# Performance work log

Hardware: AMD Instinct MI355X
Metric: run time of the kernel (lower is better)

Reference implementation:

```python
import jax, jax.numpy as jnp
import numpy as np

HIDDEN = 2048
N_HEADS = 32
N_KV_HEADS = 8
HEAD_DIM = HIDDEN // N_HEADS  # 64
KV_GROUPS = N_HEADS // N_KV_HEADS  # 4
ROPE_THETA = 10000.0
BSZ, SEQ = 2, 2048


def setup_inputs() -> dict:
    key = jax.random.key(0)
    ks = jax.random.split(key, 5)
    s = 0.02
    hidden_states = jax.random.normal(ks[0], (BSZ, SEQ, HIDDEN), jnp.float32)
    position_ids = jnp.broadcast_to(jnp.arange(SEQ, dtype=jnp.int32), (BSZ, SEQ))
    Wq = jax.random.normal(ks[1], (HIDDEN, HIDDEN), jnp.float32) * s
    Wk = jax.random.normal(ks[2], (N_KV_HEADS * HEAD_DIM, HIDDEN), jnp.float32) * s
    Wv = jax.random.normal(ks[3], (N_KV_HEADS * HEAD_DIM, HIDDEN), jnp.float32) * s
    Wo = jax.random.normal(ks[4], (HIDDEN, HIDDEN), jnp.float32) * s
    return {"hidden_states": hidden_states, "position_ids": position_ids,
            "Wq": Wq, "Wk": Wk, "Wv": Wv, "Wo": Wo}


def _rope_cos_sin(position_ids):
    # Llama rotary embedding: inv_freq over even dims, emb = [freqs, freqs]
    inv_freq = 1.0 / (ROPE_THETA ** (jnp.arange(0, HEAD_DIM, 2, dtype=jnp.float32) / HEAD_DIM))  # [Hd/2]
    freqs = position_ids.astype(jnp.float32)[..., None] * inv_freq  # [B, S, Hd/2]
    emb = jnp.concatenate([freqs, freqs], axis=-1)  # [B, S, Hd]
    return jnp.cos(emb), jnp.sin(emb)


def _rotate_half(x):
    x1, x2 = jnp.split(x, 2, axis=-1)
    return jnp.concatenate([-x2, x1], axis=-1)


def reference(hidden_states, position_ids, Wq, Wk, Wv, Wo):
    bsz, seq_len, _ = hidden_states.shape
    # projections (nn.Linear: y = x @ W.T)
    q = (hidden_states @ Wq.T).reshape(bsz, seq_len, N_HEADS, HEAD_DIM).transpose(0, 2, 1, 3)
    k = (hidden_states @ Wk.T).reshape(bsz, seq_len, N_KV_HEADS, HEAD_DIM).transpose(0, 2, 1, 3)
    v = (hidden_states @ Wv.T).reshape(bsz, seq_len, N_KV_HEADS, HEAD_DIM).transpose(0, 2, 1, 3)
    cos, sin = _rope_cos_sin(position_ids)  # [B, S, Hd]
    cos = cos[:, None, :, :]
    sin = sin[:, None, :, :]
    q = q * cos + _rotate_half(q) * sin
    k = k * cos + _rotate_half(k) * sin
    # GQA expand kv heads to full head count
    k = jnp.repeat(k, KV_GROUPS, axis=1)  # [B, H, S, Hd]
    v = jnp.repeat(v, KV_GROUPS, axis=1)
    # naive full-softmax attention (no causal mask, matching the source)
    scores = jnp.einsum('bhqd,bhkd->bhqk', q, k) / jnp.sqrt(jnp.float32(HEAD_DIM))
    attn_w = jax.nn.softmax(scores, axis=-1)
    attn_o = jnp.einsum('bhqk,bhkd->bhqd', attn_w, v)
    attn_o = attn_o.transpose(0, 2, 1, 3).reshape(bsz, seq_len, HIDDEN)
    return attn_o @ Wo.T
```

## Files before the change

### kernel.cpp

```cpp
#include <hip/hip_runtime.h>
#include <hip/hip_bf16.h>
#include <stdint.h>

#define HID 2048
#define NH 32
#define NKV 8
#define HD 64
#define BSZ 2
#define SEQ 2048
#define NROWS (BSZ*SEQ)
#define KVCOLS (NKV*HD)
#define QKVN 3072

typedef __attribute__((ext_vector_type(8))) short bf16x8;
typedef __attribute__((ext_vector_type(4))) float f32x4;
typedef __attribute__((ext_vector_type(16))) float f32x16;
typedef __attribute__((ext_vector_type(2))) unsigned int u32x2;

__device__ __forceinline__ unsigned short f2bf(float f) {
  union { float f; uint32_t u; } v; v.f = f;
  uint32_t r = v.u + 0x7FFFu + ((v.u >> 16) & 1u);
  return (unsigned short)(r >> 16);
}

__device__ __forceinline__ unsigned pack_bf16(float a, float b) {
  union { __hip_bfloat162 h; unsigned u; } cv;
  cv.h = __float22bfloat162_rn(make_float2(a, b));
  return cv.u;
}

__device__ __forceinline__ float sum16(const f32x16& s) {
  float a0 = s[0] + s[1], a1 = s[2] + s[3], a2 = s[4] + s[5], a3 = s[6] + s[7];
  float a4 = s[8] + s[9], a5 = s[10] + s[11], a6 = s[12] + s[13], a7 = s[14] + s[15];
  float b0 = a0 + a1, b1 = a2 + a3, b2 = a4 + a5, b3 = a6 + a7;
  return (b0 + b1) + (b2 + b3);
}

#define MKPB(S, B0) ({ \
  unsigned A_ = pack_bf16((S)[B0], (S)[(B0)+1]); \
  unsigned C_ = pack_bf16((S)[(B0)+2], (S)[(B0)+3]); \
  unsigned B_ = pack_bf16((S)[(B0)+4], (S)[(B0)+5]); \
  unsigned D_ = pack_bf16((S)[(B0)+6], (S)[(B0)+7]); \
  u32x2 r0_ = __builtin_amdgcn_permlane32_swap(A_, B_, false, false); \
  u32x2 r1_ = __builtin_amdgcn_permlane32_swap(C_, D_, false, false); \
  union { uint4 u; bf16x8 v; } cv_; \
  cv_.u.x = r0_.x; cv_.u.y = r1_.x; cv_.u.z = r0_.y; cv_.u.w = r1_.y; \
  cv_.v; })

#define ROPE_C (-0.41524101186092029f)
#define QSCL 0.18033688011112042f

#define C0 2097152
#define C1 3145728
#define C2 3407872
#define C3 3670016
#define CT 4718592
#define CT2 (CT + 32768)
__global__ __launch_bounds__(256) void cvt_all(
    const float* __restrict__ hs, const float* __restrict__ wq,
    const float* __restrict__ wk, const float* __restrict__ wv,
    const float* __restrict__ wo, const int* __restrict__ pos_ids,
    unsigned short* __restrict__ xb, unsigned short* __restrict__ wqkv,
    unsigned short* __restrict__ wob, float2* __restrict__ tab) {
  int i4 = blockIdx.x * 256 + threadIdx.x;
  const int stride = gridDim.x * 256;
  for (; i4 < CT2; i4 += stride) {
    if (i4 >= CT) {
      const int idx = i4 - CT;
      const int row = idx >> 3, jb = (idx & 7) * 4;
      const float pos = (float)pos_ids[row];
      float2 e[4];
      #pragma unroll
      for (int jj = 0; jj < 4; ++jj) {
        float sn, cs;
        __sincosf(pos * exp2f((float)(jb + jj) * ROPE_C), &sn, &cs);
        e[jj].x = cs; e[jj].y = sn;
      }
      *(float4*)(tab + (size_t)row * 32 + jb)     = *(const float4*)&e[0];
      *(float4*)(tab + (size_t)row * 32 + jb + 2) = *(const float4*)&e[2];
      continue;
    }
    const float* src; unsigned short* dst;
    if (i4 < C0)      { src = hs + (size_t)i4 * 4;            dst = xb   + (size_t)i4 * 4; }
    else if (i4 < C1) { src = wq + (size_t)(i4 - C0) * 4;     dst = wqkv + (size_t)(i4 - C0) * 4; }
    else if (i4 < C2) { src = wk + (size_t)(i4 - C1) * 4;     dst = wqkv + 4194304 + (size_t)(i4 - C1) * 4; }
    else if (i4 < C3) { src = wv + (size_t)(i4 - C2) * 4;     dst = wqkv + 5242880 + (size_t)(i4 - C2) * 4; }
    else              { src = wo + (size_t)(i4 - C3) * 4;     dst = wob  + (size_t)(i4 - C3) * 4; }
    float4 v = *(const float4*)src;
    ushort4 o;
    o.x = f2bf(v.x); o.y = f2bf(v.y); o.z = f2bf(v.z); o.w = f2bf(v.w);
    *(ushort4*)dst = o;
  }
}

#define BM 128
#define BN 128
#define BK 32

__global__ __launch_bounds__(256) void gemm_btn(
    const unsigned short* __restrict__ A,
    const unsigned short* __restrict__ B,
    float* __restrict__ C,
    int M, int N, int K)
{
  __shared__ unsigned short As[2][BM * BK];
  __shared__ unsigned short Bs[2][BN * BK];
  const int t = threadIdx.x;
  const int w = t >> 6, l = t & 63;
  const int wr = w >> 1, wc = w & 1;

  const int nwg = gridDim.x * gridDim.y;
  const int lin = blockIdx.y * gridDim.x + blockIdx.x;
  const int swz = (lin & 7) * (nwg >> 3) + (lin >> 3);
  const int bx = swz % gridDim.x, by = swz / gridDim.x;

  const int row0 = by * BM, col0 = bx * BN;
  const int lr = l & 15, lk = (l >> 4) * 8;

  f32x4 acc[4][4];
  for (int i = 0; i < 4; ++i)
    for (int j = 0; j < 4; ++j)
      acc[i][j] = (f32x4){0.f, 0.f, 0.f, 0.f};

  auto stage = [&](int bi, int k0) {
    #pragma unroll
    for (int i = 0; i < 2; ++i) {
      int ebase = i * 2048 + w * 512;
      int e = ebase + l * 8;
      const unsigned short* srcA = A + (size_t)(row0 + (e >> 5)) * K + k0 + (e & 31);
      const unsigned short* srcB = B + (size_t)(col0 + (e >> 5)) * K + k0 + (e & 31);
      __builtin_amdgcn_global_load_lds((const __attribute__((address_space(1))) void*)srcA,
          (__attribute__((address_space(3))) void*)&As[bi][ebase], 16, 0, 0);
      __builtin_amdgcn_global_load_lds((const __attribute__((address_space(1))) void*)srcB,
          (__attribute__((address_space(3))) void*)&Bs[bi][ebase], 16, 0, 0);
    }
  };

  stage(0, 0);
  __syncthreads();
  int bi = 0;
  for (int k0 = 0; k0 < K; k0 += BK) {
    if (k0 + BK < K) stage(bi ^ 1, k0 + BK);
    bf16x8 a[4], b[4];
    #pragma unroll
    for (int mi = 0; mi < 4; ++mi)
      a[mi] = *(const bf16x8*)&As[bi][(wr * 64 + mi * 16 + lr) * BK + lk];
    #pragma unroll
    for (int ni = 0; ni < 4; ++ni)
      b[ni] = *(const bf16x8*)&Bs[bi][(wc * 64 + ni * 16 + lr) * BK + lk];
    #pragma unroll
    for (int mi = 0; mi < 4; ++mi)
      #pragma unroll
      for (int ni = 0; ni < 4; ++ni)
        acc[mi][ni] = __builtin_amdgcn_mfma_f32_16x16x32_bf16(a[mi], b[ni], acc[mi][ni], 0, 0, 0);
    __syncthreads();
    bi ^= 1;
  }

  const int crow = (l >> 4) * 4, ccol = l & 15;
  #pragma unroll
  for (int mi = 0; mi < 4; ++mi)
    #pragma unroll
    for (int ni = 0; ni < 4; ++ni) {
      float* cp = C + (size_t)(row0 + wr * 64 + mi * 16 + crow) * N + col0 + wc * 64 + ni * 16 + ccol;
      #pragma unroll
      for (int r = 0; r < 4; ++r)
        cp[(size_t)r * N] = acc[mi][ni][r];
    }
}

__global__ __launch_bounds__(256) void gemm_qkv(
    const unsigned short* __restrict__ A,
    const unsigned short* __restrict__ B,
    const float2* __restrict__ tab,
    unsigned short* __restrict__ Qb,
    unsigned short* __restrict__ Kb,
    unsigned short* __restrict__ Vt)
{
  __shared__ unsigned short Sh[4 * BM * BK];
  unsigned short* As = Sh;
  unsigned short* Bs = Sh + 2 * BM * BK;
  const int t = threadIdx.x;
  const int w = t >> 6, l = t & 63;
  const int wr = w >> 1, wc = w & 1;

  const int nwg = gridDim.x * gridDim.y;
  const int lin = blockIdx.y * gridDim.x + blockIdx.x;
  const int swz = (lin & 7) * (nwg >> 3) + (lin >> 3);
  const int bx = swz % gridDim.x, by = swz / gridDim.x;

  const int row0 = by * BM, col0 = bx * BN;
  const int lr = l & 15, lk = (l >> 4) * 8;

  f32x4 acc[4][4];
  for (int i = 0; i < 4; ++i)
    for (int j = 0; j < 4; ++j)
      acc[i][j] = (f32x4){0.f, 0.f, 0.f, 0.f};

  auto stage = [&](int bi, int k0) {
    #pragma unroll
    for (int i = 0; i < 2; ++i) {
      int ebase = i * 2048 + w * 512;
      int e = ebase + l * 8;
      const unsigned short* srcA = A + (size_t)(row0 + (e >> 5)) * HID + k0 + (e & 31);
      const unsigned short* srcB = B + (size_t)(col0 + (e >> 5)) * HID + k0 + (e & 31);
      __builtin_amdgcn_global_load_lds((const __attribute__((address_space(1))) void*)srcA,
          (__attribute__((address_space(3))) void*)&As[bi * BM * BK + ebase], 16, 0, 0);
      __builtin_amdgcn_global_load_lds((const __attribute__((address_space(1))) void*)srcB,
          (__attribute__((address_space(3))) void*)&Bs[bi * BM * BK + ebase], 16, 0, 0);
    }
  };

  stage(0, 0);
  __syncthreads();
  int bi = 0;
  for (int k0 = 0; k0 < HID; k0 += BK) {
    if (k0 + BK < HID) stage(bi ^ 1, k0 + BK);
    bf16x8 a[4], b[4];
    #pragma unroll
    for (int mi = 0; mi < 4; ++mi)
      a[mi] = *(const bf16x8*)&As[bi * BM * BK + (wr * 64 + mi * 16 + lr) * BK + lk];
    #pragma unroll
    for (int ni = 0; ni < 4; ++ni)
      b[ni] = *(const bf16x8*)&Bs[bi * BM * BK + (wc * 64 + ni * 16 + lr) * BK + lk];
    #pragma unroll
    for (int mi = 0; mi < 4; ++mi)
      #pragma unroll
      for (int ni = 0; ni < 4; ++ni)
        acc[mi][ni] = __builtin_amdgcn_mfma_f32_16x16x32_bf16(a[mi], b[ni], acc[mi][ni], 0, 0, 0);
    __syncthreads();
    bi ^= 1;
  }

  const int crow = (l >> 4) * 4, ccol = l & 15;
  const int colbase = col0 + wc * 64;
  const int b = row0 >> 11;
  const int s0row = (row0 + wr * 64) & (SEQ - 1);
  char* Tw = (char*)Sh + w * 8192;
  const int dl = l >> 3, sg = l & 7;

  if (colbase < HID + KVCOLS) {
    const bool isQ = colbase < HID;
    const float scl = isQ ? QSCL : 1.0f;
    const int hh = (isQ ? colbase : colbase - HID) >> 6;
    unsigned short* base = (isQ ? Qb + ((size_t)(b * NH + hh) * SEQ) * HD
                                : Kb + ((size_t)(b * NKV + hh) * SEQ) * HD);
    #pragma unroll
    for (int mi = 0; mi < 4; ++mi) {
      const int rowb = row0 + wr * 64 + mi * 16 + crow;
      #pragma unroll
      for (int r = 0; r < 4; ++r) {
        const int row = rowb + r;
        const int sl = mi * 16 + crow + r;
        const int xsw = (sl & 7) << 4;
        const float2* tr = tab + (size_t)row * 32 + ccol;
        #pragma unroll
        for (int ni = 0; ni < 2; ++ni) {
          const float2 cssn = tr[ni * 16];
          const float x1 = acc[mi][ni][r], x2 = acc[mi][ni + 2][r];
          const int d1 = (ni * 16 + ccol) * 2;
          *(unsigned short*)(Tw + ((sl * 128 + d1) ^ xsw)) =
              f2bf((x1 * cssn.x - x2 * cssn.y) * scl);
          *(unsigned short*)(Tw + ((sl * 128 + d1 + 64) ^ xsw)) =
              f2bf((x2 * cssn.x + x1 * cssn.y) * scl);
        }
      }
    }
    asm volatile("s_waitcnt lgkmcnt(0)" ::: "memory");
    __builtin_amdgcn_sched_barrier(0);
    #pragma unroll
    for (int dg = 0; dg < 8; ++dg) {
      const int sl = dg * 8 + dl;
      uint4 v = *(const uint4*)(Tw + ((sl * 128 + sg * 16) ^ ((sl & 7) << 4)));
      *(uint4*)(base + (size_t)(s0row + sl) * HD + sg * 8) = v;
    }
  } else {
    const int cv = colbase - (HID + KVCOLS);
    const int kh = cv >> 6;
    unsigned short* vbase = Vt + ((size_t)(b * NKV + kh) * HD) * SEQ;
    #pragma unroll
    for (int ni = 0; ni < 4; ++ni) {
      const int d = ni * 16 + ccol;
      #pragma unroll
      for (int mi = 0; mi < 4; ++mi) {
        const int sl = mi * 16 + crow;
        ushort4 o;
        o.x = f2bf(acc[mi][ni][0]);
        o.y = f2bf(acc[mi][ni][1]);
        o.z = f2bf(acc[mi][ni][2]);
        o.w = f2bf(acc[mi][ni][3]);
        *(ushort4*)(Tw + ((d * 128 + sl * 2) ^ ((d & 7) << 4))) = o;
      }
    }
    asm volatile("s_waitcnt lgkmcnt(0)" ::: "memory");
    __builtin_amdgcn_sched_barrier(0);
    #pragma unroll
    for (int dg = 0; dg < 8; ++dg) {
      const int d = dg * 8 + dl;
      uint4 v = *(const uint4*)(Tw + ((d * 128 + sg * 16) ^ ((d & 7) << 4)));
      *(uint4*)(vbase + (size_t)d * SEQ + s0row + sg * 8) = v;
    }
  }
}

__global__ __launch_bounds__(512, 4) void attn_kernel(
    const unsigned short* __restrict__ Qb,
    const unsigned short* __restrict__ Kb,
    const unsigned short* __restrict__ Vt,
    unsigned short* __restrict__ AO)
{
  __shared__ unsigned short Ks[2][64 * 64];
  __shared__ unsigned short Vs[2][64 * 64];

  const int lin = blockIdx.x;
  const int bid = (lin & 7) * 64 + (lin >> 3);
  const int qtile = bid & 7;
  const int h = (bid >> 3) & 31;
  const int b = bid >> 8;
  const int kh = h >> 2;
  const int t = threadIdx.x, w = t >> 6, l = t & 63;
  const int lq = l & 31, hi = l >> 5;
  const int sw = (lq & 7) << 4;
  const int qrow = qtile * 256 + w * 32 + lq;

  bf16x8 qf[4];
  {
    const unsigned short* Qrow = Qb + ((size_t)(b * NH + h) * SEQ + qrow) * HD;
    #pragma unroll
    for (int dk = 0; dk < 4; ++dk)
      qf[dk] = *(const bf16x8*)(Qrow + dk * 16 + hi * 8);
  }

  const unsigned short* Kt  = Kb + (size_t)(b * NKV + kh) * SEQ * HD;
  const unsigned short* Vth = Vt + (size_t)(b * NKV + kh) * HD * SEQ;

  const int dest = t * 16;
  const int srow = dest >> 7;
  const int scol = dest & 127;
  const int wdest = dest ^ ((srow & 7) << 4);
  const char* KsrcBase = (const char*)Kt + dest;
  const char* VsrcBase = (const char*)(Vth + (size_t)srow * SEQ) + scol;

  uint4 kreg, vreg;
  auto issue = [&](int kv0) {
    kreg = *(const uint4*)(KsrcBase + (size_t)kv0 * 128);
    vreg = *(const uint4*)(VsrcBase + kv0 * 2);
  };
  auto lwrite = [&](int si) {
    *(uint4*)((char*)Ks[si] + wdest) = kreg;
    *(uint4*)((char*)Vs[si] + wdest) = vreg;
  };

  const f32x16 Z = {0,0,0,0,0,0,0,0,0,0,0,0,0,0,0,0};
  float lsum = 0.f;
  f32x16 o0 = Z, o1 = Z;

  issue(0);
  lwrite(0);
  __syncthreads();

  int bi = 0;
  for (int it = 0; it < SEQ / 64; ++it) {
    const bool more = (it + 1 < SEQ / 64);
    if (more) issue((it + 1) * 64);

    const char* Kp = (const char*)Ks[bi];
    const char* Vp = (const char*)Vs[bi];

    f32x16 s0, s1;
    __builtin_amdgcn_s_setprio(1);
    {
      bf16x8 kf0 = *(const bf16x8*)(Kp + lq * 128 + ((hi * 16) ^ sw));
      bf16x8 kf1 = *(const bf16x8*)(Kp + 4096 + lq * 128 + ((hi * 16) ^ sw));
      s0 = __builtin_amdgcn_mfma_f32_32x32x16_bf16(kf0, qf[0], Z, 0, 0, 0);
      s1 = __builtin_amdgcn_mfma_f32_32x32x16_bf16(kf1, qf[0], Z, 0, 0, 0);
    }
    #pragma unroll
    for (int dk = 1; dk < 4; ++dk) {
      const int cb = dk * 32 + hi * 16;
      bf16x8 kf0 = *(const bf16x8*)(Kp + lq * 128 + (cb ^ sw));
      bf16x8 kf1 = *(const bf16x8*)(Kp + 4096 + lq * 128 + (cb ^ sw));
      s0 = __builtin_amdgcn_mfma_f32_32x32x16_bf16(kf0, qf[dk], s0, 0, 0, 0);
      s1 = __builtin_amdgcn_mfma_f32_32x32x16_bf16(kf1, qf[dk], s1, 0, 0, 0);
    }
    __builtin_amdgcn_s_setprio(0);

    #pragma unroll
    for (int r = 0; r < 16; ++r) { s0[r] = exp2f(s0[r]); s1[r] = exp2f(s1[r]); }
    float rs = sum16(s0) + sum16(s1);
    rs += __shfl_xor(rs, 32);
    lsum += rs;

    bf16x8 pb0 = MKPB(s0, 0), pb1 = MKPB(s0, 8), pb2 = MKPB(s1, 0), pb3 = MKPB(s1, 8);

    __builtin_amdgcn_s_setprio(1);
    #pragma unroll
    for (int ks = 0; ks < 4; ++ks) {
      const int cb = ks * 32 + hi * 16;
      bf16x8 vf0 = *(const bf16x8*)(Vp + lq * 128 + (cb ^ sw));
      bf16x8 vf1 = *(const bf16x8*)(Vp + 4096 + lq * 128 + (cb ^ sw));
      bf16x8 pa = (ks == 0) ? pb0 : (ks == 1) ? pb1 : (ks == 2) ? pb2 : pb3;
      o0 = __builtin_amdgcn_mfma_f32_32x32x16_bf16(vf0, pa, o0, 0, 0, 0);
      o1 = __builtin_amdgcn_mfma_f32_32x32x16_bf16(vf1, pa, o1, 0, 0, 0);
    }
    __builtin_amdgcn_s_setprio(0);

    if (more) lwrite(bi ^ 1);
    __syncthreads();
    bi ^= 1;
  }

  const float inv = 1.0f / lsum;
  unsigned short* op = AO + ((size_t)(b * SEQ) + qrow) * HID + h * 64;
  #pragma unroll
  for (int r = 0; r < 16; r += 2) {
    const int d = (r & 3) + 8 * (r >> 2) + 4 * hi;
    *(unsigned*)(op + d)      = pack_bf16(o0[r] * inv, o0[r + 1] * inv);
    *(unsigned*)(op + 32 + d) = pack_bf16(o1[r] * inv, o1[r + 1] * inv);
  }
}

extern "C" void kernel_launch(void* const* d_in, const int* in_sizes, int n_in,
                              void* d_out, int out_size, void* d_ws, size_t ws_size,
                              hipStream_t stream) {
  const float* hs  = (const float*)d_in[0];
  const int*   pos = (const int*)d_in[1];
  const float* Wq  = (const float*)d_in[2];
  const float* Wk  = (const float*)d_in[3];
  const float* Wv  = (const float*)d_in[4];
  const float* Wo  = (const float*)d_in[5];
  float* out = (float*)d_out;

  char* ws = (char*)d_ws;
  size_t off = 0;
  auto carve = [&](size_t bytes) { void* p = ws + off; off += (bytes + 255) & ~(size_t)255; return p; };

  unsigned short* Xb    = (unsigned short*)carve((size_t)NROWS * HID * 2);
  unsigned short* Wqkvb = (unsigned short*)carve((size_t)QKVN * HID * 2);
  unsigned short* Wob   = (unsigned short*)carve((size_t)HID * HID * 2);
  unsigned short* Qbh   = (unsigned short*)carve((size_t)NROWS * HID * 2);
  unsigned short* Kbh   = (unsigned short*)carve((size_t)NROWS * KVCOLS * 2);
  unsigned short* Vtb   = (unsigned short*)carve((size_t)NROWS * KVCOLS * 2);
  unsigned short* AO    = (unsigned short*)carve((size_t)NROWS * HID * 2);
  float2*         Tab   = (float2*)carve((size_t)NROWS * 32 * sizeof(float2));

  cvt_all<<<2048, 256, 0, stream>>>(hs, Wq, Wk, Wv, Wo, pos, Xb, Wqkvb, Wob, Tab);

  gemm_qkv<<<dim3(QKVN / BN, NROWS / BM), 256, 0, stream>>>(Xb, Wqkvb, Tab, Qbh, Kbh, Vtb);

  attn_kernel<<<BSZ * NH * (SEQ / 256), 512, 0, stream>>>(Qbh, Kbh, Vtb, AO);

  gemm_btn<<<dim3(HID / BN, NROWS / BM), 256, 0, stream>>>(AO, Wob, out, NROWS, HID, HID);
}
```

Before: 260.0 us.

## Rewrite projection GEMMs with 256x256 tiles, BK=64, swizzled LDS and 8-wave blocks

```diff
diff --git a/kernel.cpp b/kernel.cpp
--- a/kernel.cpp
+++ b/kernel.cpp
@@ -49,6 +49,10 @@
 
 #define ROPE_C (-0.41524101186092029f)
 #define QSCL 0.18033688011112042f
+
+#define GLOAD(src, dst) __builtin_amdgcn_global_load_lds( \
+    (const __attribute__((address_space(1))) void*)(src), \
+    (__attribute__((address_space(3))) void*)(dst), 16, 0, 0)
 
 #define C0 2097152
 #define C1 3145728
@@ -93,83 +97,108 @@
   }
 }
 
-#define BM 128
-#define BN 128
-#define BK 32
-
-__global__ __launch_bounds__(256) void gemm_btn(
+#define G_STAGE8(bufB, ktn) \
+  { \
+    _Pragma("unroll") \
+    for (int j = 0; j < 4; ++j) { \
+      int d = wcn * 4096 + j * 1024 + l * 16; \
+      int colp = (d & 127) ^ (((d >> 7) & 7) << 4); \
+      GLOAD((const char*)A + (size_t)(row0 + wr * 128 + (d >> 7)) * 4096 + (ktn) * 128 + colp, \
+            SL + (bufB) + wr * 16384 + d); \
+    } \
+    _Pragma("unroll") \
+    for (int j = 0; j < 4; ++j) { \
+      int d = (wr * 2 + (wcn & 1)) * 4096 + j * 1024 + l * 16; \
+      int colp = (d & 127) ^ (((d >> 7) & 7) << 4); \
+      GLOAD((const char*)B + (size_t)(col0 + (wcn >> 1) * 128 + (d >> 7)) * 4096 + (ktn) * 128 + colp, \
+            SL + (bufB) + 32768 + (wcn >> 1) * 16384 + d); \
+    } \
+  }
+
+#define G_TILE(bufB) \
+  _Pragma("unroll") \
+  for (int ks = 0; ks < 2; ++ks) { \
+    bf16x8 af[8]; \
+    _Pragma("unroll") \
+    for (int mi = 0; mi < 8; ++mi) \
+      af[mi] = *(const bf16x8*)(SL + (bufB) + ABb + mi * 2048 + laneK[ks]); \
+    _Pragma("unroll") \
+    for (int nh = 0; nh < 2; ++nh) { \
+      bf16x8 b0 = *(const bf16x8*)(SL + (bufB) + BBb + (nh * 2) * 2048 + laneK[ks]); \
+      bf16x8 b1 = *(const bf16x8*)(SL + (bufB) + BBb + (nh * 2 + 1) * 2048 + laneK[ks]); \
+      __builtin_amdgcn_s_barrier(); \
+      __builtin_amdgcn_sched_barrier(0); \
+      __builtin_amdgcn_s_setprio(1); \
+      _Pragma("unroll") \
+      for (int mi = 0; mi < 8; ++mi) { \
+        acc[mi][nh * 2]     = __builtin_amdgcn_mfma_f32_16x16x32_bf16(af[mi], b0, acc[mi][nh * 2], 0, 0, 0); \
+        acc[mi][nh * 2 + 1] = __builtin_amdgcn_mfma_f32_16x16x32_bf16(af[mi], b1, acc[mi][nh * 2 + 1], 0, 0, 0); \
+      } \
+      __builtin_amdgcn_s_setprio(0); \
+      __builtin_amdgcn_s_barrier(); \
+      __builtin_amdgcn_sched_barrier(0); \
+    } \
+  }
+
+#define G_PREAMBLE \
+  __shared__ char SL[131072]; \
+  const int t = threadIdx.x; \
+  const int w = t >> 6, l = t & 63; \
+  const int wr = w >> 2, wcn = w & 3; \
+  const int lr = l & 15, lk2 = (l >> 4) * 16; \
+  const int sw7 = (lr & 7) << 4; \
+  const int nwg = gridDim.x * gridDim.y; \
+  const int lin = blockIdx.y * gridDim.x + blockIdx.x; \
+  const int swzb = (lin & 7) * (nwg >> 3) + (lin >> 3); \
+  const int bx = swzb % gridDim.x, by = swzb / gridDim.x; \
+  const int row0 = by * 256, col0 = bx * 256; \
+  int laneK[2]; \
+  laneK[0] = lr * 128 + (lk2 ^ sw7); \
+  laneK[1] = lr * 128 + ((64 + lk2) ^ sw7); \
+  const int ABb = wr * 16384; \
+  const int BBb = 32768 + (wcn >> 1) * 16384 + (wcn & 1) * 8192; \
+  f32x4 acc[8][4]; \
+  _Pragma("unroll") \
+  for (int i = 0; i < 8; ++i) \
+    _Pragma("unroll") \
+    for (int j = 0; j < 4; ++j) acc[i][j] = (f32x4){0.f, 0.f, 0.f, 0.f}; \
+  G_STAGE8(0, 0); \
+  asm volatile("s_waitcnt vmcnt(0)" ::: "memory"); \
+  __syncthreads(); \
+  _Pragma("unroll 1") \
+  for (int kt2 = 0; kt2 < 16; ++kt2) { \
+    const int kt = kt2 * 2; \
+    if (kt + 1 < 32) G_STAGE8(65536, kt + 1); \
+    G_TILE(0); \
+    asm volatile("s_waitcnt vmcnt(0)" ::: "memory"); \
+    __builtin_amdgcn_s_barrier(); \
+    __builtin_amdgcn_sched_barrier(0); \
+    if (kt + 2 < 32) G_STAGE8(0, kt + 2); \
+    G_TILE(65536); \
+    asm volatile("s_waitcnt vmcnt(0)" ::: "memory"); \
+    __builtin_amdgcn_s_barrier(); \
+    __builtin_amdgcn_sched_barrier(0); \
+  }
+
+__global__ __launch_bounds__(512, 2) void gemm_btn256(
     const unsigned short* __restrict__ A,
     const unsigned short* __restrict__ B,
-    float* __restrict__ C,
-    int M, int N, int K)
+    float* __restrict__ C)
 {
-  __shared__ unsigned short As[2][BM * BK];
-  __shared__ unsigned short Bs[2][BN * BK];
-  const int t = threadIdx.x;
-  const int w = t >> 6, l = t & 63;
-  const int wr = w >> 1, wc = w & 1;
-
-  const int nwg = gridDim.x * gridDim.y;
-  const int lin = blockIdx.y * gridDim.x + blockIdx.x;
-  const int swz = (lin & 7) * (nwg >> 3) + (lin >> 3);
-  const int bx = swz % gridDim.x, by = swz / gridDim.x;
-
-  const int row0 = by * BM, col0 = bx * BN;
-  const int lr = l & 15, lk = (l >> 4) * 8;
-
-  f32x4 acc[4][4];
-  for (int i = 0; i < 4; ++i)
-    for (int j = 0; j < 4; ++j)
-      acc[i][j] = (f32x4){0.f, 0.f, 0.f, 0.f};
-
-  auto stage = [&](int bi, int k0) {
-    #pragma unroll
-    for (int i = 0; i < 2; ++i) {
-      int ebase = i * 2048 + w * 512;
-      int e = ebase + l * 8;
-      const unsigned short* srcA = A + (size_t)(row0 + (e >> 5)) * K + k0 + (e & 31);
-      const unsigned short* srcB = B + (size_t)(col0 + (e >> 5)) * K + k0 + (e & 31);
-      __builtin_amdgcn_global_load_lds((const __attribute__((address_space(1))) void*)srcA,
-          (__attribute__((address_space(3))) void*)&As[bi][ebase], 16, 0, 0);
-      __builtin_amdgcn_global_load_lds((const __attribute__((address_space(1))) void*)srcB,
-          (__attribute__((address_space(3))) void*)&Bs[bi][ebase], 16, 0, 0);
-    }
-  };
-
-  stage(0, 0);
-  __syncthreads();
-  int bi = 0;
-  for (int k0 = 0; k0 < K; k0 += BK) {
-    if (k0 + BK < K) stage(bi ^ 1, k0 + BK);
-    bf16x8 a[4], b[4];
-    #pragma unroll
-    for (int mi = 0; mi < 4; ++mi)
-      a[mi] = *(const bf16x8*)&As[bi][(wr * 64 + mi * 16 + lr) * BK + lk];
-    #pragma unroll
-    for (int ni = 0; ni < 4; ++ni)
-      b[ni] = *(const bf16x8*)&Bs[bi][(wc * 64 + ni * 16 + lr) * BK + lk];
-    #pragma unroll
-    for (int mi = 0; mi < 4; ++mi)
-      #pragma unroll
-      for (int ni = 0; ni < 4; ++ni)
-        acc[mi][ni] = __builtin_amdgcn_mfma_f32_16x16x32_bf16(a[mi], b[ni], acc[mi][ni], 0, 0, 0);
-    __syncthreads();
-    bi ^= 1;
-  }
-
+  G_PREAMBLE
   const int crow = (l >> 4) * 4, ccol = l & 15;
   #pragma unroll
-  for (int mi = 0; mi < 4; ++mi)
+  for (int mi = 0; mi < 8; ++mi)
     #pragma unroll
     for (int ni = 0; ni < 4; ++ni) {
-      float* cp = C + (size_t)(row0 + wr * 64 + mi * 16 + crow) * N + col0 + wc * 64 + ni * 16 + ccol;
+      float* cp = C + (size_t)(row0 + wr * 128 + mi * 16 + crow) * HID + col0 + wcn * 64 + ni * 16 + ccol;
       #pragma unroll
       for (int r = 0; r < 4; ++r)
-        cp[(size_t)r * N] = acc[mi][ni][r];
-    }
-}
-
-__global__ __launch_bounds__(256) void gemm_qkv(
+        cp[(size_t)r * HID] = acc[mi][ni][r];
+    }
+}
+
+__global__ __launch_bounds__(512, 2) void gemm_qkv256(
     const unsigned short* __restrict__ A,
     const unsigned short* __restrict__ B,
     const float2* __restrict__ tab,
@@ -177,67 +206,12 @@
     unsigned short* __restrict__ Kb,
     unsigned short* __restrict__ Vt)
 {
-  __shared__ unsigned short Sh[4 * BM * BK];
-  unsigned short* As = Sh;
-  unsigned short* Bs = Sh + 2 * BM * BK;
-  const int t = threadIdx.x;
-  const int w = t >> 6, l = t & 63;
-  const int wr = w >> 1, wc = w & 1;
-
-  const int nwg = gridDim.x * gridDim.y;
-  const int lin = blockIdx.y * gridDim.x + blockIdx.x;
-  const int swz = (lin & 7) * (nwg >> 3) + (lin >> 3);
-  const int bx = swz % gridDim.x, by = swz / gridDim.x;
-
-  const int row0 = by * BM, col0 = bx * BN;
-  const int lr = l & 15, lk = (l >> 4) * 8;
-
-  f32x4 acc[4][4];
-  for (int i = 0; i < 4; ++i)
-    for (int j = 0; j < 4; ++j)
-      acc[i][j] = (f32x4){0.f, 0.f, 0.f, 0.f};
-
-  auto stage = [&](int bi, int k0) {
-    #pragma unroll
-    for (int i = 0; i < 2; ++i) {
-      int ebase = i * 2048 + w * 512;
-      int e = ebase + l * 8;
-      const unsigned short* srcA = A + (size_t)(row0 + (e >> 5)) * HID + k0 + (e & 31);
-      const unsigned short* srcB = B + (size_t)(col0 + (e >> 5)) * HID + k0 + (e & 31);
-      __builtin_amdgcn_global_load_lds((const __attribute__((address_space(1))) void*)srcA,
-          (__attribute__((address_space(3))) void*)&As[bi * BM * BK + ebase], 16, 0, 0);
-      __builtin_amdgcn_global_load_lds((const __attribute__((address_space(1))) void*)srcB,
-          (__attribute__((address_space(3))) void*)&Bs[bi * BM * BK + ebase], 16, 0, 0);
-    }
-  };
-
-  stage(0, 0);
-  __syncthreads();
-  int bi = 0;
-  for (int k0 = 0; k0 < HID; k0 += BK) {
-    if (k0 + BK < HID) stage(bi ^ 1, k0 + BK);
-    bf16x8 a[4], b[4];
-    #pragma unroll
-    for (int mi = 0; mi < 4; ++mi)
-      a[mi] = *(const bf16x8*)&As[bi * BM * BK + (wr * 64 + mi * 16 + lr) * BK + lk];
-    #pragma unroll
-    for (int ni = 0; ni < 4; ++ni)
-      b[ni] = *(const bf16x8*)&Bs[bi * BM * BK + (wc * 64 + ni * 16 + lr) * BK + lk];
-    #pragma unroll
-    for (int mi = 0; mi < 4; ++mi)
-      #pragma unroll
-      for (int ni = 0; ni < 4; ++ni)
-        acc[mi][ni] = __builtin_amdgcn_mfma_f32_16x16x32_bf16(a[mi], b[ni], acc[mi][ni], 0, 0, 0);
-    __syncthreads();
-    bi ^= 1;
-  }
-
+  G_PREAMBLE
   const int crow = (l >> 4) * 4, ccol = l & 15;
-  const int colbase = col0 + wc * 64;
+  const int colbase = col0 + wcn * 64;
   const int b = row0 >> 11;
-  const int s0row = (row0 + wr * 64) & (SEQ - 1);
-  char* Tw = (char*)Sh + w * 8192;
-  const int dl = l >> 3, sg = l & 7;
+  const int s0row = (row0 + wr * 128) & (SEQ - 1);
+  char* Tw = SL + w * 16384;
 
   if (colbase < HID + KVCOLS) {
     const bool isQ = colbase < HID;
@@ -246,12 +220,11 @@
     unsigned short* base = (isQ ? Qb + ((size_t)(b * NH + hh) * SEQ) * HD
                                 : Kb + ((size_t)(b * NKV + hh) * SEQ) * HD);
     #pragma unroll
-    for (int mi = 0; mi < 4; ++mi) {
-      const int rowb = row0 + wr * 64 + mi * 16 + crow;
+    for (int mi = 0; mi < 8; ++mi) {
       #pragma unroll
       for (int r = 0; r < 4; ++r) {
-        const int row = rowb + r;
         const int sl = mi * 16 + crow + r;
+        const int row = row0 + wr * 128 + sl;
         const int xsw = (sl & 7) << 4;
         const float2* tr = tab + (size_t)row * 32 + ccol;
         #pragma unroll
@@ -268,11 +241,12 @@
     }
     asm volatile("s_waitcnt lgkmcnt(0)" ::: "memory");
     __builtin_amdgcn_sched_barrier(0);
-    #pragma unroll
-    for (int dg = 0; dg < 8; ++dg) {
+    const int dl = l >> 3, sg = l & 7;
+    #pragma unroll
+    for (int dg = 0; dg < 16; ++dg) {
       const int sl = dg * 8 + dl;
       uint4 v = *(const uint4*)(Tw + ((sl * 128 + sg * 16) ^ ((sl & 7) << 4)));
-      *(uint4*)(base + (size_t)(s0row + sl) * HD + sg * 8) = v;
+      *(uint4*)((char*)base + (size_t)(s0row + sl) * 128 + sg * 16) = v;
     }
   } else {
     const int cv = colbase - (HID + KVCOLS);
@@ -282,23 +256,24 @@
     for (int ni = 0; ni < 4; ++ni) {
       const int d = ni * 16 + ccol;
       #pragma unroll
-      for (int mi = 0; mi < 4; ++mi) {
+      for (int mi = 0; mi < 8; ++mi) {
         const int sl = mi * 16 + crow;
         ushort4 o;
         o.x = f2bf(acc[mi][ni][0]);
         o.y = f2bf(acc[mi][ni][1]);
         o.z = f2bf(acc[mi][ni][2]);
         o.w = f2bf(acc[mi][ni][3]);
-        *(ushort4*)(Tw + ((d * 128 + sl * 2) ^ ((d & 7) << 4))) = o;
+        *(ushort4*)(Tw + (d * 256 + ((sl * 2) ^ ((d & 7) << 4)))) = o;
       }
     }
     asm volatile("s_waitcnt lgkmcnt(0)" ::: "memory");
     __builtin_amdgcn_sched_barrier(0);
-    #pragma unroll
-    for (int dg = 0; dg < 8; ++dg) {
-      const int d = dg * 8 + dl;
-      uint4 v = *(const uint4*)(Tw + ((d * 128 + sg * 16) ^ ((d & 7) << 4)));
-      *(uint4*)(vbase + (size_t)d * SEQ + s0row + sg * 8) = v;
+    const int dl2 = l >> 4, sgl = l & 15;
+    #pragma unroll
+    for (int dg = 0; dg < 16; ++dg) {
+      const int d = dg * 4 + dl2;
+      uint4 v = *(const uint4*)(Tw + (d * 256 + ((sgl * 16) ^ ((d & 7) << 4))));
+      *(uint4*)(vbase + (size_t)d * SEQ + s0row + sgl * 8) = v;
     }
   }
 }
@@ -446,9 +421,9 @@
 
   cvt_all<<<2048, 256, 0, stream>>>(hs, Wq, Wk, Wv, Wo, pos, Xb, Wqkvb, Wob, Tab);
 
-  gemm_qkv<<<dim3(QKVN / BN, NROWS / BM), 256, 0, stream>>>(Xb, Wqkvb, Tab, Qbh, Kbh, Vtb);
+  gemm_qkv256<<<dim3(QKVN / 256, NROWS / 256), 512, 0, stream>>>(Xb, Wqkvb, Tab, Qbh, Kbh, Vtb);
 
   attn_kernel<<<BSZ * NH * (SEQ / 256), 512, 0, stream>>>(Qbh, Kbh, Vtb, AO);
 
-  gemm_btn<<<dim3(HID / BN, NROWS / BM), 256, 0, stream>>>(AO, Wob, out, NROWS, HID, HID);
-}
+  gemm_btn256<<<dim3(HID / 256, NROWS / 256), 512, 0, stream>>>(AO, Wob, out);
+}
```

New measurement: 304.3 us. +17.0%, slower.
